# Kernel tuning notes

Measured on AMD Instinct MI355X. Metric: run time of the kernel, lower is better.

## Reference

```python
import jax, jax.numpy as jnp
import numpy as np

CUTOFF_FREQ = 4000.0
SAMPLE_RATE = 48000.0
FILTER_ORDER = 6


def _butter_lowpass(order, wn):
    """Digital Butterworth low-pass (b, a), matching scipy.signal.butter(order, wn, 'low')."""
    fs = 2.0
    warped = 2.0 * fs * np.tan(np.pi * wn / fs)
    # Analog Butterworth prototype poles (buttap)
    m = np.arange(-order + 1, order, 2)
    p = -np.exp(1j * np.pi * m / (2 * order))
    k = 1.0
    # lp2lp: scale poles by warped cutoff
    p = warped * p
    k = k * warped ** order
    # Bilinear transform (fs=2); zeros map to -1
    fs2 = 2.0 * fs
    pz = (fs2 + p) / (fs2 - p)
    kz = k * np.real(1.0 / np.prod(fs2 - p))
    zz = -np.ones(order)
    b = (kz * np.poly(zz)).real
    a = np.poly(pz).real
    return b.astype(np.float32), a.astype(np.float32)

_B, _A = _butter_lowpass(FILTER_ORDER, CUTOFF_FREQ / (0.5 * SAMPLE_RATE))


def _lfilter(x):
    """IIR filter along last axis, direct-form II transposed (matches scipy.signal.lfilter
    with zero initial state). x: [B, T] -> [B, T]."""
    b = jnp.asarray(_B, x.dtype)
    a = jnp.asarray(_A, x.dtype)
    n = b.shape[0] - 1  # filter order
    b0, bi, ai = b[0], b[1:], a[1:]

    def step(z, x_t):  # z: [B, n], x_t: [B]
        y = b0 * x_t + z[:, 0]
        z_shift = jnp.concatenate([z[:, 1:], jnp.zeros_like(z[:, :1])], axis=1)
        z_new = z_shift + bi[None, :] * x_t[:, None] - ai[None, :] * y[:, None]
        return z_new, y

    z0 = jnp.zeros((x.shape[0], n), x.dtype)
    _, ys = jax.lax.scan(step, z0, x.T)  # ys: [T, B]
    return ys.T


def setup_inputs() -> dict:
    key = jax.random.key(0)
    k1, k2 = jax.random.split(key)
    B, T = 96, 131072
    output = jax.random.normal(k1, (B, T), dtype=jnp.float32)
    target = jax.random.normal(k2, (B, T), dtype=jnp.float32)
    return {"output": output, "target": target}


def reference(output, target):
    filtered_output = _lfilter(output)
    filtered_target = _lfilter(target)
    return jnp.mean(jnp.abs(filtered_output - filtered_target))
```

## Files before the change

### kernel.cpp

```cpp
#include <hip/hip_runtime.h>
#include <cmath>
#include <complex>

#define T_LEN   131072
#define B_ROWS  96
#define CHUNK   32
#define WARM    64
#define SEG     8192
#define NSEG    (T_LEN / SEG)
#define NLDS    (SEG + WARM)
#define NF4     (NLDS / 4)
#define BLOCK   256
#define WPT     24
#define GRID    (B_ROWS * NSEG)

struct Coefs {
  float b0, b1, b2, b3, b4, b5, b6;
  float a1, a2, a3, a4, a5, a6;
  float invN;
};

__device__ __forceinline__ int swz(int f) { return f ^ ((f >> 3) & 7); }

#define LP_STEP(x, ACC)                                  \
  {                                                      \
    float y = fmaf(cf.b0, (x), z0);                      \
    ACC;                                                 \
    z0 = fmaf(-cf.a1, y, fmaf(cf.b1, (x), z1));          \
    z1 = fmaf(-cf.a2, y, fmaf(cf.b2, (x), z2));          \
    z2 = fmaf(-cf.a3, y, fmaf(cf.b3, (x), z3));          \
    z3 = fmaf(-cf.a4, y, fmaf(cf.b4, (x), z4));          \
    z4 = fmaf(-cf.a5, y, fmaf(cf.b5, (x), z5));          \
    z5 = fmaf(-cf.a6, y, cf.b6 * (x));                   \
  }

__global__ __launch_bounds__(BLOCK, 4) void lp_mae_kernel(
    const float* __restrict__ out_p, const float* __restrict__ tgt_p,
    float* __restrict__ partial, Coefs cf)
{
  __shared__ float4 xs[NF4];
  __shared__ float red[BLOCK / 64];

  const int blk = blockIdx.x;
  const int row = blk >> 4;
  const int s   = blk & (NSEG - 1);

  const size_t segbase = (size_t)row * T_LEN + (size_t)s * SEG;
  const float4* po = (const float4*)(out_p + segbase - WARM);
  const float4* pt = (const float4*)(tgt_p + segbase - WARM);

  for (int g = threadIdx.x; g < NF4; g += BLOCK) {
    float4 d;
    if (s == 0 && g < (WARM / 4)) {
      d = make_float4(0.f, 0.f, 0.f, 0.f);
    } else {
      float4 xo = po[g];
      float4 xt = pt[g];
      d.x = xo.x - xt.x; d.y = xo.y - xt.y;
      d.z = xo.z - xt.z; d.w = xo.w - xt.w;
    }
    xs[swz(g)] = d;
  }
  __syncthreads();

  float4 w[WPT];
  #pragma unroll
  for (int j = 0; j < WPT; ++j)
    w[j] = xs[swz(threadIdx.x * 8 + j)];

  float z0 = 0.f, z1 = 0.f, z2 = 0.f, z3 = 0.f, z4 = 0.f, z5 = 0.f;
  float sum = 0.f;

  #pragma unroll
  for (int j = 0; j < WARM / 4; ++j) {
    LP_STEP(w[j].x, );
    LP_STEP(w[j].y, );
    LP_STEP(w[j].z, );
    LP_STEP(w[j].w, );
  }
  #pragma unroll
  for (int j = WARM / 4; j < WPT; ++j) {
    LP_STEP(w[j].x, sum += fabsf(y));
    LP_STEP(w[j].y, sum += fabsf(y));
    LP_STEP(w[j].z, sum += fabsf(y));
    LP_STEP(w[j].w, sum += fabsf(y));
  }

  #pragma unroll
  for (int off = 32; off > 0; off >>= 1)
    sum += __shfl_down(sum, off);
  if ((threadIdx.x & 63) == 0)
    red[threadIdx.x >> 6] = sum;
  __syncthreads();
  if (threadIdx.x == 0)
    partial[blk] = red[0] + red[1] + red[2] + red[3];
}

__global__ __launch_bounds__(BLOCK) void lp_reduce_kernel(
    const float* __restrict__ partial, float* __restrict__ dout, float invN)
{
  __shared__ float red[BLOCK / 64];
  float sum = 0.f;
  for (int i = threadIdx.x; i < GRID; i += BLOCK)
    sum += partial[i];
  #pragma unroll
  for (int off = 32; off > 0; off >>= 1)
    sum += __shfl_down(sum, off);
  if ((threadIdx.x & 63) == 0)
    red[threadIdx.x >> 6] = sum;
  __syncthreads();
  if (threadIdx.x == 0)
    dout[0] = (red[0] + red[1] + red[2] + red[3]) * invN;
}

extern "C" void kernel_launch(void* const* d_in, const int* in_sizes, int n_in,
                              void* d_out, int out_size, void* d_ws, size_t ws_size,
                              hipStream_t stream) {
  (void)in_sizes; (void)n_in; (void)ws_size; (void)out_size;

  const float* out_p = (const float*)d_in[0];
  const float* tgt_p = (const float*)d_in[1];
  float* dout = (float*)d_out;
  float* partial = (float*)d_ws;

  using cd = std::complex<double>;
  const int order = 6;
  const double wn = 4000.0 / 24000.0;
  const double fs = 2.0;
  const double warped = 2.0 * fs * std::tan(M_PI * wn / fs);

  cd p[6];
  for (int k = 0; k < order; ++k) {
    int m = -order + 1 + 2 * k;
    p[k] = -std::exp(cd(0.0, M_PI * m / (2.0 * order))) * warped;
  }
  double kgain = std::pow(warped, (double)order);
  const double fs2 = 2.0 * fs;

  cd pz[6];
  cd prodden(1.0, 0.0);
  for (int k = 0; k < order; ++k) {
    pz[k] = (fs2 + p[k]) / (fs2 - p[k]);
    prodden *= (fs2 - p[k]);
  }
  double kz = kgain * std::real(1.0 / prodden);

  const double binom[7] = {1, 6, 15, 20, 15, 6, 1};
  double bd[7];
  for (int i = 0; i < 7; ++i) bd[i] = kz * binom[i];

  cd ac[7];
  ac[0] = cd(1.0, 0.0);
  for (int i = 1; i < 7; ++i) ac[i] = cd(0.0, 0.0);
  for (int k = 0; k < order; ++k)
    for (int i = k + 1; i >= 1; --i)
      ac[i] = ac[i] - pz[k] * ac[i - 1];

  Coefs cf;
  cf.b0 = (float)bd[0]; cf.b1 = (float)bd[1]; cf.b2 = (float)bd[2];
  cf.b3 = (float)bd[3]; cf.b4 = (float)bd[4]; cf.b5 = (float)bd[5];
  cf.b6 = (float)bd[6];
  cf.a1 = (float)std::real(ac[1]); cf.a2 = (float)std::real(ac[2]);
  cf.a3 = (float)std::real(ac[3]); cf.a4 = (float)std::real(ac[4]);
  cf.a5 = (float)std::real(ac[5]); cf.a6 = (float)std::real(ac[6]);
  cf.invN = 1.0f / (float)((double)B_ROWS * (double)T_LEN);

  lp_mae_kernel<<<GRID, BLOCK, 0, stream>>>(out_p, tgt_p, partial, cf);
  lp_reduce_kernel<<<1, BLOCK, 0, stream>>>(partial, dout, cf.invN);
}
```

Measured before the change: 127.0 us.

## Store input differences in LDS as bf16 and shorten the filter warm-up window

Each block now packs the output-minus-target differences into bf16 pairs in shared memory, which halves the LDS footprint. That allows 8 blocks per CU instead of 4. The warm-up prefix for each 32-sample chunk drops from 64 to 48 samples, so less filter work is wasted per thread. Samples are read and unpacked one 8-element slot at a time rather than all kept in registers. Rounding the inputs to bf16 and using a shorter warm-up both add numerical error to the mean absolute error, which could exceed the tolerance.

```diff
diff --git a/kernel.cpp b/kernel.cpp
--- a/kernel.cpp
+++ b/kernel.cpp
@@ -5,14 +5,15 @@
 #define T_LEN   131072
 #define B_ROWS  96
 #define CHUNK   32
-#define WARM    64
+#define WARM    48
 #define SEG     8192
 #define NSEG    (T_LEN / SEG)
 #define NLDS    (SEG + WARM)
-#define NF4     (NLDS / 4)
+#define NSLOT   (NLDS / 8)
 #define BLOCK   256
-#define WPT     24
 #define GRID    (B_ROWS * NSEG)
+#define WSLOT   ((WARM + CHUNK) / 8)
+#define ZSLOT   (WARM / 8)
 
 struct Coefs {
   float b0, b1, b2, b3, b4, b5, b6;
@@ -20,7 +21,17 @@
   float invN;
 };
 
-__device__ __forceinline__ int swz(int f) { return f ^ ((f >> 3) & 7); }
+__device__ __forceinline__ int swz8(int s) { return s ^ ((s >> 3) & 7); }
+
+__device__ __forceinline__ unsigned bf16rne(float x) {
+  unsigned b = __float_as_uint(x);
+  return (b + 0x7FFFu + ((b >> 16) & 1u)) >> 16;
+}
+__device__ __forceinline__ unsigned packdiff(float a0, float b0, float a1, float b1) {
+  return bf16rne(a0 - b0) | (bf16rne(a1 - b1) << 16);
+}
+#define UNLO(u) __uint_as_float((u) << 16)
+#define UNHI(u) __uint_as_float((u) & 0xFFFF0000u)
 
 #define LP_STEP(x, ACC)                                  \
   {                                                      \
@@ -34,65 +45,79 @@
     z5 = fmaf(-cf.a6, y, cf.b6 * (x));                   \
   }
 
-__global__ __launch_bounds__(BLOCK, 4) void lp_mae_kernel(
+__global__ __launch_bounds__(BLOCK, 8) void lp_mae_kernel(
     const float* __restrict__ out_p, const float* __restrict__ tgt_p,
     float* __restrict__ partial, Coefs cf)
 {
-  __shared__ float4 xs[NF4];
+  __shared__ uint4 xs[NSLOT];
   __shared__ float red[BLOCK / 64];
 
+  const int tid = threadIdx.x;
   const int blk = blockIdx.x;
   const int row = blk >> 4;
   const int s   = blk & (NSEG - 1);
+  const bool first = (s == 0);
 
   const size_t segbase = (size_t)row * T_LEN + (size_t)s * SEG;
   const float4* po = (const float4*)(out_p + segbase - WARM);
   const float4* pt = (const float4*)(tgt_p + segbase - WARM);
 
-  for (int g = threadIdx.x; g < NF4; g += BLOCK) {
-    float4 d;
-    if (s == 0 && g < (WARM / 4)) {
-      d = make_float4(0.f, 0.f, 0.f, 0.f);
+  #pragma unroll
+  for (int r = 0; r < 4; ++r) {
+    const int g = r * BLOCK + tid;
+    uint4 v;
+    if (first && g < ZSLOT) {
+      v = make_uint4(0u, 0u, 0u, 0u);
     } else {
-      float4 xo = po[g];
-      float4 xt = pt[g];
-      d.x = xo.x - xt.x; d.y = xo.y - xt.y;
-      d.z = xo.z - xt.z; d.w = xo.w - xt.w;
+      float4 a0 = po[2 * g], a1 = po[2 * g + 1];
+      float4 b0 = pt[2 * g], b1 = pt[2 * g + 1];
+      v.x = packdiff(a0.x, b0.x, a0.y, b0.y);
+      v.y = packdiff(a0.z, b0.z, a0.w, b0.w);
+      v.z = packdiff(a1.x, b1.x, a1.y, b1.y);
+      v.w = packdiff(a1.z, b1.z, a1.w, b1.w);
     }
-    xs[swz(g)] = d;
+    xs[swz8(g)] = v;
+  }
+  if (tid < (NSLOT - 4 * BLOCK)) {
+    const int g = 4 * BLOCK + tid;
+    float4 a0 = po[2 * g], a1 = po[2 * g + 1];
+    float4 b0 = pt[2 * g], b1 = pt[2 * g + 1];
+    uint4 v;
+    v.x = packdiff(a0.x, b0.x, a0.y, b0.y);
+    v.y = packdiff(a0.z, b0.z, a0.w, b0.w);
+    v.z = packdiff(a1.x, b1.x, a1.y, b1.y);
+    v.w = packdiff(a1.z, b1.z, a1.w, b1.w);
+    xs[swz8(g)] = v;
   }
   __syncthreads();
 
-  float4 w[WPT];
-  #pragma unroll
-  for (int j = 0; j < WPT; ++j)
-    w[j] = xs[swz(threadIdx.x * 8 + j)];
-
+  const int base = tid * 4;
   float z0 = 0.f, z1 = 0.f, z2 = 0.f, z3 = 0.f, z4 = 0.f, z5 = 0.f;
   float sum = 0.f;
 
   #pragma unroll
-  for (int j = 0; j < WARM / 4; ++j) {
-    LP_STEP(w[j].x, );
-    LP_STEP(w[j].y, );
-    LP_STEP(w[j].z, );
-    LP_STEP(w[j].w, );
-  }
-  #pragma unroll
-  for (int j = WARM / 4; j < WPT; ++j) {
-    LP_STEP(w[j].x, sum += fabsf(y));
-    LP_STEP(w[j].y, sum += fabsf(y));
-    LP_STEP(w[j].z, sum += fabsf(y));
-    LP_STEP(w[j].w, sum += fabsf(y));
+  for (int j = 0; j < WSLOT; ++j) {
+    const uint4 v = xs[swz8(base + j)];
+    if (j < WSLOT - CHUNK / 8) {
+      LP_STEP(UNLO(v.x), );  LP_STEP(UNHI(v.x), );
+      LP_STEP(UNLO(v.y), );  LP_STEP(UNHI(v.y), );
+      LP_STEP(UNLO(v.z), );  LP_STEP(UNHI(v.z), );
+      LP_STEP(UNLO(v.w), );  LP_STEP(UNHI(v.w), );
+    } else {
+      LP_STEP(UNLO(v.x), sum += fabsf(y));  LP_STEP(UNHI(v.x), sum += fabsf(y));
+      LP_STEP(UNLO(v.y), sum += fabsf(y));  LP_STEP(UNHI(v.y), sum += fabsf(y));
+      LP_STEP(UNLO(v.z), sum += fabsf(y));  LP_STEP(UNHI(v.z), sum += fabsf(y));
+      LP_STEP(UNLO(v.w), sum += fabsf(y));  LP_STEP(UNHI(v.w), sum += fabsf(y));
+    }
   }
 
   #pragma unroll
   for (int off = 32; off > 0; off >>= 1)
     sum += __shfl_down(sum, off);
-  if ((threadIdx.x & 63) == 0)
-    red[threadIdx.x >> 6] = sum;
+  if ((tid & 63) == 0)
+    red[tid >> 6] = sum;
   __syncthreads();
-  if (threadIdx.x == 0)
+  if (tid == 0)
     partial[blk] = red[0] + red[1] + red[2] + red[3];
 }
 
```

After: 120.4 us. 1.05x faster.
